# Performance work log

Hardware: AMD Instinct MI355X
Metric: run time of the kernel (lower is better)

The kernel has to match this reference:

```python
import jax, jax.numpy as jnp
import numpy as np

N_NODES, N_EDGES, D_FEAT, HIDDEN, N_CLASSES = 100000, 3200000, 128, 16, 40


def setup_inputs() -> dict:
    key = jax.random.key(0)
    ks = jax.random.split(key, 6)
    x = jax.random.normal(ks[0], (N_NODES, D_FEAT), dtype=jnp.float32)
    edge_index = jax.random.randint(ks[1], (2, N_EDGES), 0, N_NODES, dtype=jnp.int32)
    # SAGEConv params: lin_l (aggregated neighbors, with bias), lin_r (root, no bias)
    W_l = jax.random.normal(ks[2], (D_FEAT, HIDDEN), dtype=jnp.float32) / np.sqrt(D_FEAT)
    b_l = jnp.zeros((HIDDEN,), jnp.float32)
    W_r = jax.random.normal(ks[3], (D_FEAT, HIDDEN), dtype=jnp.float32) / np.sqrt(D_FEAT)
    # final Linear(hidden, num_classes)
    W3 = jax.random.normal(ks[4], (HIDDEN, N_CLASSES), dtype=jnp.float32) / np.sqrt(HIDDEN)
    b3 = jnp.zeros((N_CLASSES,), jnp.float32)
    return {"x": x, "edge_index": edge_index, "W_l": W_l, "b_l": b_l,
            "W_r": W_r, "W3": W3, "b3": b3}


def reference(x, edge_index, W_l, b_l, W_r, W3, b3):
    N = x.shape[0]
    src, dst = edge_index[0], edge_index[1]
    # mean aggregation of source features onto target nodes (PyG source_to_target)
    agg = jax.ops.segment_sum(x[src], dst, num_segments=N)            # [N, F]
    deg = jax.ops.segment_sum(jnp.ones_like(dst, dtype=x.dtype), dst, num_segments=N)
    mean = agg / jnp.maximum(deg, 1.0)[:, None]                        # zero-in-degree -> 0
    # SAGEConv: lin_l(mean) + lin_r(x)
    h = mean @ W_l + b_l + x @ W_r                                     # [N, 16]
    h = jax.nn.relu(h)
    logits = h @ W3 + b3                                               # [N, C]
    return jax.nn.log_softmax(logits, axis=1)
```

## Files before the change

### kernel.cpp

```cpp
#include <hip/hip_runtime.h>
#include <hip/hip_bf16.h>

#define D_FEAT 128
#define HIDDEN 16
#define NCLS 40
#define EPB 4096
#define QSCALE 32.0f
#define QBIAS  8.0f

typedef unsigned int uint;

__device__ __forceinline__ void fma4(float4& a, float s, const float4 w) {
  a.x += s * w.x; a.y += s * w.y; a.z += s * w.z; a.w += s * w.w;
}

__global__ __launch_bounds__(256) void pass1_kernel(
    const int* __restrict__ src, const int* __restrict__ dst,
    int* __restrict__ gcur1, int* __restrict__ buf1,
    int E, int C, int R1) {
  __shared__ int lh[32], loff[32], gbase[32];
  __shared__ int lbuf[EPB];
  __shared__ int ldst[EPB];
  int tid = threadIdx.x;
  if (tid < 32) lh[tid] = 0;
  __syncthreads();

  int base = blockIdx.x * EPB;
  int key[16], rnk[16], rec[16];
#pragma unroll
  for (int j = 0; j < 16; ++j) {
    int e = base + j * 256 + tid;
    bool ok = e < E;
    int d = ok ? dst[e] : 0;
    int s = ok ? src[e] : 0;
    key[j] = ok ? (d >> 12) : -1;
    rec[j] = s | ((d & 4095) << 17);
    if (ok) rnk[j] = atomicAdd(&lh[key[j]], 1);
  }
  __syncthreads();

  if (tid < 64) {
    int v = (tid < 32) ? lh[tid] : 0;
    int inc = v;
#pragma unroll
    for (int dd = 1; dd < 32; dd <<= 1) {
      int t = __shfl_up(inc, dd);
      if ((int)tid >= dd) inc += t;
    }
    if (tid < 32) {
      loff[tid] = inc - v;
      gbase[tid] = (v && tid < C) ? atomicAdd(&gcur1[tid], v) : 0;
    }
  }
  __syncthreads();

#pragma unroll
  for (int j = 0; j < 16; ++j) {
    if (key[j] >= 0) {
      int p = loff[key[j]] + rnk[j];
      lbuf[p] = rec[j];
      int gp = gbase[key[j]] + rnk[j];
      ldst[p] = (gp < R1) ? key[j] * R1 + gp : -1;
    }
  }
  __syncthreads();

  int tot = min(EPB, E - base);
  for (int i = tid; i < tot; i += 256) {
    int di = ldst[i];
    if (di >= 0) buf1[di] = lbuf[i];
  }
}

__global__ __launch_bounds__(256) void p2lin_kernel(
    const int* __restrict__ buf1, const int* __restrict__ gcur1,
    int* __restrict__ gcur, int* __restrict__ packed,
    int C, int R1, int RF, int chunks, int nb2,
    const float* __restrict__ x,
    const float* __restrict__ Wl, const float* __restrict__ Wr,
    uint* __restrict__ ylb, float* __restrict__ yr, int N) {
  __shared__ __align__(16) char smem[16896];
  int tid = threadIdx.x;

  if ((int)blockIdx.x < nb2) {
    int* lbuf  = (int*)smem;
    int* lh    = (int*)(smem + 16384);
    int* loff  = lh + 32;
    int* gbase = loff + 32;

    int c = blockIdx.x / chunks;
    int chunk = blockIdx.x - c * chunks;
    int cnt1 = min(gcur1[c], R1);
    int base = chunk * EPB;
    int tot = cnt1 - base;
    if (tot <= 0) return;
    tot = min(tot, EPB);

    if (tid < 32) lh[tid] = 0;
    __syncthreads();

    const int* in = buf1 + (size_t)c * R1 + base;
    int key[16], rnk[16], rec[16];
#pragma unroll
    for (int j = 0; j < 16; ++j) {
      int i = j * 256 + tid;
      bool ok = i < tot;
      int r = ok ? in[i] : 0;
      key[j] = ok ? ((r >> 24) & 31) : -1;
      rec[j] = r;
      if (ok) rnk[j] = atomicAdd(&lh[key[j]], 1);
    }
    __syncthreads();

    if (tid < 64) {
      int v = (tid < 32) ? lh[tid] : 0;
      int inc = v;
#pragma unroll
      for (int dd = 1; dd < 32; dd <<= 1) {
        int t = __shfl_up(inc, dd);
        if ((int)tid >= dd) inc += t;
      }
      if (tid < 32) {
        loff[tid] = inc - v;
        gbase[tid] = v ? atomicAdd(&gcur[c * 32 + tid], v) : 0;
      }
    }
    __syncthreads();

#pragma unroll
    for (int j = 0; j < 16; ++j)
      if (key[j] >= 0) lbuf[loff[key[j]] + rnk[j]] = rec[j];
    __syncthreads();

    for (int i = tid; i < tot; i += 256) {
      int r = lbuf[i];
      int k = (r >> 24) & 31;
      int gp = gbase[k] + (i - loff[k]);
      if (gp < RF) {
        int d12 = (r >> 17) & 4095;
        packed[(size_t)(c * 32 + k) * RF + gp] =
            (r & 0x1FFFF) | ((d12 & 127) << 20);
      }
    }
  } else {
    float* sW = (float*)smem;
    const float4* sWf4 = (const float4*)smem;

    for (int i = tid; i < 4096; i += 256) {
      int k = i >> 5, c = i & 31;
      sW[i] = (c < 16) ? Wl[k * 16 + c] : Wr[k * 16 + (c - 16)];
    }
    __syncthreads();

    int row0 = ((int)blockIdx.x - nb2) * 128;
    int quad = tid & 7, rg = tid >> 3;
    int r0 = row0 + rg * 4;
    int rr0 = min(r0 + 0, N - 1), rr1 = min(r0 + 1, N - 1);
    int rr2 = min(r0 + 2, N - 1), rr3 = min(r0 + 3, N - 1);
    const float* xp0 = x + (size_t)rr0 * D_FEAT;
    const float* xp1 = x + (size_t)rr1 * D_FEAT;
    const float* xp2 = x + (size_t)rr2 * D_FEAT;
    const float* xp3 = x + (size_t)rr3 * D_FEAT;

    float4 acc0 = {0,0,0,0}, acc1 = {0,0,0,0}, acc2 = {0,0,0,0}, acc3 = {0,0,0,0};
#pragma unroll 4
    for (int k4 = 0; k4 < 32; ++k4) {
      float4 x0 = *(const float4*)(xp0 + k4 * 4);
      float4 x1 = *(const float4*)(xp1 + k4 * 4);
      float4 x2 = *(const float4*)(xp2 + k4 * 4);
      float4 x3 = *(const float4*)(xp3 + k4 * 4);
      float4 w0 = sWf4[(k4 * 4 + 0) * 8 + quad];
      fma4(acc0, x0.x, w0); fma4(acc1, x1.x, w0);
      fma4(acc2, x2.x, w0); fma4(acc3, x3.x, w0);
      float4 w1 = sWf4[(k4 * 4 + 1) * 8 + quad];
      fma4(acc0, x0.y, w1); fma4(acc1, x1.y, w1);
      fma4(acc2, x2.y, w1); fma4(acc3, x3.y, w1);
      float4 w2 = sWf4[(k4 * 4 + 2) * 8 + quad];
      fma4(acc0, x0.z, w2); fma4(acc1, x1.z, w2);
      fma4(acc2, x2.z, w2); fma4(acc3, x3.z, w2);
      float4 w3 = sWf4[(k4 * 4 + 3) * 8 + quad];
      fma4(acc0, x0.w, w3); fma4(acc1, x1.w, w3);
      fma4(acc2, x2.w, w3); fma4(acc3, x3.w, w3);
    }

    float4 accs[4] = {acc0, acc1, acc2, acc3};
    if (quad < 4) {
#pragma unroll
      for (int r = 0; r < 4; ++r) {
        if (r0 + r < N) {
          float4 a = accs[r];
          int q0 = __float2int_rn((fminf(fmaxf(a.x, -7.9f), 7.9f) + QBIAS) * QSCALE);
          int q1 = __float2int_rn((fminf(fmaxf(a.y, -7.9f), 7.9f) + QBIAS) * QSCALE);
          int q2 = __float2int_rn((fminf(fmaxf(a.z, -7.9f), 7.9f) + QBIAS) * QSCALE);
          int q3 = __float2int_rn((fminf(fmaxf(a.w, -7.9f), 7.9f) + QBIAS) * QSCALE);
          uint2 pk;
          pk.x = (uint)q0 | ((uint)q1 << 16);
          pk.y = (uint)q2 | ((uint)q3 << 16);
          *(uint2*)(ylb + (size_t)(r0 + r) * 8 + quad * 2) = pk;
        }
      }
    } else {
#pragma unroll
      for (int r = 0; r < 4; ++r) {
        if (r0 + r < N)
          *(float4*)(yr + (size_t)(r0 + r) * 16 + (quad - 4) * 4) = accs[r];
      }
    }
  }
}

__global__ __launch_bounds__(1024) void baggrf_kernel(
    const uint* __restrict__ ylb, const int* __restrict__ packed,
    const int* __restrict__ gcur, const float* __restrict__ yr,
    const float* __restrict__ bl, const float* __restrict__ W3,
    const float* __restrict__ b3, float* __restrict__ out,
    int N, int RF) {
  __shared__ uint sagg[128 * 9];
  __shared__ int sdeg[128];
  __shared__ float syr[128 * 16];
  __shared__ float sW3[16 * NCLS];
  __shared__ float sb3[NCLS];
  __shared__ float sbl[16];
  int tid = threadIdx.x;
  int b = blockIdx.x;
  int node0 = b * 128;

  for (int i = tid; i < 128 * 9; i += 1024) sagg[i] = 0u;
  if (tid < 128) sdeg[tid] = 0;
  if (tid >= 384 && tid < 1024) sW3[tid - 384] = W3[tid - 384];
  if (tid < NCLS) sb3[tid] = b3[tid];
  if (tid >= 64 && tid < 80) sbl[tid - 64] = bl[tid - 64];
  __syncthreads();

  int cnt = min(gcur[b], RF);
  int lo = b * RF, hi = lo + cnt;
  for (int e = lo + tid; e < hi; e += 2048) {
    int eb = e + 1024;
    bool has2 = eb < hi;
    int p0 = packed[e];
    int p1 = packed[has2 ? eb : e];
    int s0 = p0 & 0xFFFFF, d0 = (p0 >> 20) & 127;
    int s1 = p1 & 0xFFFFF, d1 = (p1 >> 20) & 127;
    const uint4* q0 = (const uint4*)(ylb + (size_t)s0 * 8);
    const uint4* q1 = (const uint4*)(ylb + (size_t)s1 * 8);
    uint4 a0 = q0[0], a1 = q0[1];
    uint4 b0 = q1[0], b1 = q1[1];

    uint* ip0 = &sagg[d0 * 9];
    atomicAdd(ip0 + 0, a0.x); atomicAdd(ip0 + 1, a0.y);
    atomicAdd(ip0 + 2, a0.z); atomicAdd(ip0 + 3, a0.w);
    atomicAdd(ip0 + 4, a1.x); atomicAdd(ip0 + 5, a1.y);
    atomicAdd(ip0 + 6, a1.z); atomicAdd(ip0 + 7, a1.w);
    atomicAdd(&sdeg[d0], 1);
    if (has2) {
      uint* ip1 = &sagg[d1 * 9];
      atomicAdd(ip1 + 0, b0.x); atomicAdd(ip1 + 1, b0.y);
      atomicAdd(ip1 + 2, b0.z); atomicAdd(ip1 + 3, b0.w);
      atomicAdd(ip1 + 4, b1.x); atomicAdd(ip1 + 5, b1.y);
      atomicAdd(ip1 + 6, b1.z); atomicAdd(ip1 + 7, b1.w);
      atomicAdd(&sdeg[d1], 1);
    }
  }

  int nvalid = min(128, N - node0);
  if (nvalid > 0) {
    int tot16 = nvalid * 16;
    for (int i = tid; i < tot16; i += 1024)
      syr[i] = yr[(size_t)node0 * 16 + i];
  }
  __syncthreads();

  int node = tid >> 3, q = tid & 7;
  int n = node0 + node;
  if (n < N) {
    int dg = sdeg[node];
    float bsub = (QBIAS * QSCALE) * (float)dg;
    float inv = 1.0f / (QSCALE * fmaxf((float)dg, 1.0f));
    float h[16];
#pragma unroll
    for (int j = 0; j < 8; ++j) {
      uint s = sagg[node * 9 + j];
      float v0 = ((float)(s & 0xFFFFu) - bsub) * inv;
      float v1 = ((float)(s >> 16) - bsub) * inv;
      h[2 * j]     = fmaxf(v0 + sbl[2 * j]     + syr[node * 16 + 2 * j], 0.f);
      h[2 * j + 1] = fmaxf(v1 + sbl[2 * j + 1] + syr[node * 16 + 2 * j + 1], 0.f);
    }
    float lg[5];
#pragma unroll
    for (int j = 0; j < 5; ++j) lg[j] = sb3[q * 5 + j];
#pragma unroll
    for (int k = 0; k < 16; ++k) {
      float hv = h[k];
#pragma unroll
      for (int j = 0; j < 5; ++j) lg[j] += hv * sW3[k * NCLS + q * 5 + j];
    }
    float m = lg[0];
#pragma unroll
    for (int j = 1; j < 5; ++j) m = fmaxf(m, lg[j]);
#pragma unroll
    for (int dd = 1; dd < 8; dd <<= 1) m = fmaxf(m, __shfl_xor(m, dd));
    float s = 0.f;
#pragma unroll
    for (int j = 0; j < 5; ++j) s += __expf(lg[j] - m);
#pragma unroll
    for (int dd = 1; dd < 8; dd <<= 1) s += __shfl_xor(s, dd);
    float lse = m + __logf(s);
    float* op = out + (size_t)n * NCLS + q * 5;
#pragma unroll
    for (int j = 0; j < 5; ++j) op[j] = lg[j] - lse;
  }
}

extern "C" void kernel_launch(void* const* d_in, const int* in_sizes, int n_in,
                              void* d_out, int out_size, void* d_ws, size_t ws_size,
                              hipStream_t stream) {
  const float* x   = (const float*)d_in[0];
  const int* eidx  = (const int*)d_in[1];
  const float* Wl  = (const float*)d_in[2];
  const float* bl  = (const float*)d_in[3];
  const float* Wr  = (const float*)d_in[4];
  const float* W3  = (const float*)d_in[5];
  const float* b3  = (const float*)d_in[6];
  float* out = (float*)d_out;

  int N = in_sizes[0] / D_FEAT;
  int E = in_sizes[1] / 2;
  const int* src = eidx;
  const int* dst = eidx + E;

  int C = (N + 4095) >> 12;
  int chunks = (E / C) / EPB + 2;
  int R1 = chunks * EPB;
  int Bf = C * 32;
  int B = (N + 127) >> 7;
  long long m = (long long)E * 128 / N;
  int RF = (int)((m + m / 8 + 511) / 512 * 512);

  size_t n16 = (size_t)N * 16;
  uint* ylb   = (uint*)d_ws;
  float* yr   = (float*)(ylb + (size_t)N * 8);
  int* gcur   = (int*)(yr + n16);
  int* gcur1  = gcur + Bf;
  int* buf1   = gcur1 + C;
  int* packed = buf1 + (size_t)C * R1;

  hipMemsetAsync(gcur, 0, (size_t)(Bf + C) * sizeof(int), stream);

  int nb1 = (E + EPB - 1) / EPB;
  pass1_kernel<<<nb1, 256, 0, stream>>>(src, dst, gcur1, buf1, E, C, R1);

  int nb2 = C * chunks;
  int nblin = (N + 127) / 128;
  p2lin_kernel<<<nb2 + nblin, 256, 0, stream>>>(buf1, gcur1, gcur, packed,
                                                C, R1, RF, chunks, nb2,
                                                x, Wl, Wr, ylb, yr, N);

  baggrf_kernel<<<B, 1024, 0, stream>>>(ylb, packed, gcur, yr, bl, W3, b3,
                                        out, N, RF);
}
```

Before: 97.83 us.

## Co-schedule linear projection with pass1 sort and unroll aggregation loop to four edges

Moves the dense x@W projection blocks out of the pass-2 launch and into the pass-1 bucketing launch, so the projection runs alongside the first radix partition rather than the second. Pass 1 now keeps each record's bucket key in a byte array in shared memory, which cuts its shared-memory footprint from two EPB int arrays. The final aggregation loop now handles four edges per thread per iteration instead of two, giving more outstanding gathers. The costs are higher register pressure in the aggregation kernel and a different per-kernel balance across the three launches.

```diff
diff --git a/kernel.cpp b/kernel.cpp
--- a/kernel.cpp
+++ b/kernel.cpp
@@ -14,100 +14,35 @@
   a.x += s * w.x; a.y += s * w.y; a.z += s * w.z; a.w += s * w.w;
 }
 
-__global__ __launch_bounds__(256) void pass1_kernel(
+__global__ __launch_bounds__(256) void p1lin_kernel(
     const int* __restrict__ src, const int* __restrict__ dst,
     int* __restrict__ gcur1, int* __restrict__ buf1,
-    int E, int C, int R1) {
-  __shared__ int lh[32], loff[32], gbase[32];
-  __shared__ int lbuf[EPB];
-  __shared__ int ldst[EPB];
-  int tid = threadIdx.x;
-  if (tid < 32) lh[tid] = 0;
-  __syncthreads();
-
-  int base = blockIdx.x * EPB;
-  int key[16], rnk[16], rec[16];
-#pragma unroll
-  for (int j = 0; j < 16; ++j) {
-    int e = base + j * 256 + tid;
-    bool ok = e < E;
-    int d = ok ? dst[e] : 0;
-    int s = ok ? src[e] : 0;
-    key[j] = ok ? (d >> 12) : -1;
-    rec[j] = s | ((d & 4095) << 17);
-    if (ok) rnk[j] = atomicAdd(&lh[key[j]], 1);
-  }
-  __syncthreads();
-
-  if (tid < 64) {
-    int v = (tid < 32) ? lh[tid] : 0;
-    int inc = v;
-#pragma unroll
-    for (int dd = 1; dd < 32; dd <<= 1) {
-      int t = __shfl_up(inc, dd);
-      if ((int)tid >= dd) inc += t;
-    }
-    if (tid < 32) {
-      loff[tid] = inc - v;
-      gbase[tid] = (v && tid < C) ? atomicAdd(&gcur1[tid], v) : 0;
-    }
-  }
-  __syncthreads();
-
-#pragma unroll
-  for (int j = 0; j < 16; ++j) {
-    if (key[j] >= 0) {
-      int p = loff[key[j]] + rnk[j];
-      lbuf[p] = rec[j];
-      int gp = gbase[key[j]] + rnk[j];
-      ldst[p] = (gp < R1) ? key[j] * R1 + gp : -1;
-    }
-  }
-  __syncthreads();
-
-  int tot = min(EPB, E - base);
-  for (int i = tid; i < tot; i += 256) {
-    int di = ldst[i];
-    if (di >= 0) buf1[di] = lbuf[i];
-  }
-}
-
-__global__ __launch_bounds__(256) void p2lin_kernel(
-    const int* __restrict__ buf1, const int* __restrict__ gcur1,
-    int* __restrict__ gcur, int* __restrict__ packed,
-    int C, int R1, int RF, int chunks, int nb2,
+    int E, int C, int R1, int nb1,
     const float* __restrict__ x,
     const float* __restrict__ Wl, const float* __restrict__ Wr,
     uint* __restrict__ ylb, float* __restrict__ yr, int N) {
-  __shared__ __align__(16) char smem[16896];
+  __shared__ __align__(16) char smem[20880];
   int tid = threadIdx.x;
 
-  if ((int)blockIdx.x < nb2) {
+  if ((int)blockIdx.x < nb1) {
     int* lbuf  = (int*)smem;
-    int* lh    = (int*)(smem + 16384);
+    unsigned char* skey = (unsigned char*)(smem + 16384);
+    int* lh    = (int*)(smem + 20480);
     int* loff  = lh + 32;
-    int* gbase = loff + 32;
-
-    int c = blockIdx.x / chunks;
-    int chunk = blockIdx.x - c * chunks;
-    int cnt1 = min(gcur1[c], R1);
-    int base = chunk * EPB;
-    int tot = cnt1 - base;
-    if (tot <= 0) return;
-    tot = min(tot, EPB);
-
+    int* gbase = loff + 33;
     if (tid < 32) lh[tid] = 0;
     __syncthreads();
 
-    const int* in = buf1 + (size_t)c * R1 + base;
+    int base = blockIdx.x * EPB;
     int key[16], rnk[16], rec[16];
 #pragma unroll
     for (int j = 0; j < 16; ++j) {
-      int i = j * 256 + tid;
-      bool ok = i < tot;
-      int r = ok ? in[i] : 0;
-      key[j] = ok ? ((r >> 24) & 31) : -1;
-      rec[j] = r;
+      int e = base + j * 256 + tid;
+      bool ok = e < E;
+      int d = ok ? dst[e] : 0;
+      int s = ok ? src[e] : 0;
+      key[j] = ok ? (d >> 12) : -1;
+      rec[j] = s | ((d & 4095) << 17);
       if (ok) rnk[j] = atomicAdd(&lh[key[j]], 1);
     }
     __syncthreads();
@@ -122,25 +57,27 @@
       }
       if (tid < 32) {
         loff[tid] = inc - v;
-        gbase[tid] = v ? atomicAdd(&gcur[c * 32 + tid], v) : 0;
-      }
-    }
-    __syncthreads();
-
-#pragma unroll
-    for (int j = 0; j < 16; ++j)
-      if (key[j] >= 0) lbuf[loff[key[j]] + rnk[j]] = rec[j];
-    __syncthreads();
-
+        gbase[tid] = (v && tid < C) ? atomicAdd(&gcur1[tid], v) : 0;
+      }
+    }
+    __syncthreads();
+
+#pragma unroll
+    for (int j = 0; j < 16; ++j) {
+      if (key[j] >= 0) {
+        int p = loff[key[j]] + rnk[j];
+        lbuf[p] = rec[j];
+        skey[p] = (unsigned char)key[j];
+      }
+    }
+    __syncthreads();
+
+    int tot = min(EPB, E - base);
     for (int i = tid; i < tot; i += 256) {
       int r = lbuf[i];
-      int k = (r >> 24) & 31;
+      int k = skey[i];
       int gp = gbase[k] + (i - loff[k]);
-      if (gp < RF) {
-        int d12 = (r >> 17) & 4095;
-        packed[(size_t)(c * 32 + k) * RF + gp] =
-            (r & 0x1FFFF) | ((d12 & 127) << 20);
-      }
+      if (gp < R1) buf1[(size_t)k * R1 + gp] = r;
     }
   } else {
     float* sW = (float*)smem;
@@ -152,7 +89,7 @@
     }
     __syncthreads();
 
-    int row0 = ((int)blockIdx.x - nb2) * 128;
+    int row0 = ((int)blockIdx.x - nb1) * 128;
     int quad = tid & 7, rg = tid >> 3;
     int r0 = row0 + rg * 4;
     int rr0 = min(r0 + 0, N - 1), rr1 = min(r0 + 1, N - 1);
@@ -209,6 +146,70 @@
   }
 }
 
+__global__ __launch_bounds__(256) void pass2_kernel(
+    const int* __restrict__ buf1, const int* __restrict__ gcur1,
+    int* __restrict__ gcur, int* __restrict__ packed,
+    int C, int R1, int RF, int chunks) {
+  __shared__ int lbuf[EPB];
+  __shared__ int lh[32], loff[32], gbase[32];
+
+  int c = blockIdx.x / chunks;
+  int chunk = blockIdx.x - c * chunks;
+  int cnt1 = min(gcur1[c], R1);
+  int base = chunk * EPB;
+  int tot = cnt1 - base;
+  if (tot <= 0) return;
+  tot = min(tot, EPB);
+
+  int tid = threadIdx.x;
+  if (tid < 32) lh[tid] = 0;
+  __syncthreads();
+
+  const int* in = buf1 + (size_t)c * R1 + base;
+  int key[16], rnk[16], rec[16];
+#pragma unroll
+  for (int j = 0; j < 16; ++j) {
+    int i = j * 256 + tid;
+    bool ok = i < tot;
+    int r = ok ? in[i] : 0;
+    key[j] = ok ? ((r >> 24) & 31) : -1;
+    rec[j] = r;
+    if (ok) rnk[j] = atomicAdd(&lh[key[j]], 1);
+  }
+  __syncthreads();
+
+  if (tid < 64) {
+    int v = (tid < 32) ? lh[tid] : 0;
+    int inc = v;
+#pragma unroll
+    for (int dd = 1; dd < 32; dd <<= 1) {
+      int t = __shfl_up(inc, dd);
+      if ((int)tid >= dd) inc += t;
+    }
+    if (tid < 32) {
+      loff[tid] = inc - v;
+      gbase[tid] = v ? atomicAdd(&gcur[c * 32 + tid], v) : 0;
+    }
+  }
+  __syncthreads();
+
+#pragma unroll
+  for (int j = 0; j < 16; ++j)
+    if (key[j] >= 0) lbuf[loff[key[j]] + rnk[j]] = rec[j];
+  __syncthreads();
+
+  for (int i = tid; i < tot; i += 256) {
+    int r = lbuf[i];
+    int k = (r >> 24) & 31;
+    int gp = gbase[k] + (i - loff[k]);
+    if (gp < RF) {
+      int d12 = (r >> 17) & 4095;
+      packed[(size_t)(c * 32 + k) * RF + gp] =
+          (r & 0x1FFFF) | ((d12 & 127) << 20);
+    }
+  }
+}
+
 __global__ __launch_bounds__(1024) void baggrf_kernel(
     const uint* __restrict__ ylb, const int* __restrict__ packed,
     const int* __restrict__ gcur, const float* __restrict__ yr,
@@ -234,17 +235,25 @@
 
   int cnt = min(gcur[b], RF);
   int lo = b * RF, hi = lo + cnt;
-  for (int e = lo + tid; e < hi; e += 2048) {
-    int eb = e + 1024;
-    bool has2 = eb < hi;
-    int p0 = packed[e];
-    int p1 = packed[has2 ? eb : e];
+  for (int e0 = lo + tid; e0 < hi; e0 += 4096) {
+    int e1 = e0 + 1024, e2 = e0 + 2048, e3 = e0 + 3072;
+    bool h1 = e1 < hi, h2 = e2 < hi, h3 = e3 < hi;
+    int p0 = packed[e0];
+    int p1 = packed[h1 ? e1 : e0];
+    int p2 = packed[h2 ? e2 : e0];
+    int p3 = packed[h3 ? e3 : e0];
     int s0 = p0 & 0xFFFFF, d0 = (p0 >> 20) & 127;
     int s1 = p1 & 0xFFFFF, d1 = (p1 >> 20) & 127;
+    int s2 = p2 & 0xFFFFF, d2 = (p2 >> 20) & 127;
+    int s3 = p3 & 0xFFFFF, d3 = (p3 >> 20) & 127;
     const uint4* q0 = (const uint4*)(ylb + (size_t)s0 * 8);
     const uint4* q1 = (const uint4*)(ylb + (size_t)s1 * 8);
+    const uint4* q2 = (const uint4*)(ylb + (size_t)s2 * 8);
+    const uint4* q3 = (const uint4*)(ylb + (size_t)s3 * 8);
     uint4 a0 = q0[0], a1 = q0[1];
     uint4 b0 = q1[0], b1 = q1[1];
+    uint4 c0 = q2[0], c1 = q2[1];
+    uint4 e4 = q3[0], e5 = q3[1];
 
     uint* ip0 = &sagg[d0 * 9];
     atomicAdd(ip0 + 0, a0.x); atomicAdd(ip0 + 1, a0.y);
@@ -252,13 +261,29 @@
     atomicAdd(ip0 + 4, a1.x); atomicAdd(ip0 + 5, a1.y);
     atomicAdd(ip0 + 6, a1.z); atomicAdd(ip0 + 7, a1.w);
     atomicAdd(&sdeg[d0], 1);
-    if (has2) {
-      uint* ip1 = &sagg[d1 * 9];
-      atomicAdd(ip1 + 0, b0.x); atomicAdd(ip1 + 1, b0.y);
-      atomicAdd(ip1 + 2, b0.z); atomicAdd(ip1 + 3, b0.w);
-      atomicAdd(ip1 + 4, b1.x); atomicAdd(ip1 + 5, b1.y);
-      atomicAdd(ip1 + 6, b1.z); atomicAdd(ip1 + 7, b1.w);
+    if (h1) {
+      uint* ip = &sagg[d1 * 9];
+      atomicAdd(ip + 0, b0.x); atomicAdd(ip + 1, b0.y);
+      atomicAdd(ip + 2, b0.z); atomicAdd(ip + 3, b0.w);
+      atomicAdd(ip + 4, b1.x); atomicAdd(ip + 5, b1.y);
+      atomicAdd(ip + 6, b1.z); atomicAdd(ip + 7, b1.w);
       atomicAdd(&sdeg[d1], 1);
+    }
+    if (h2) {
+      uint* ip = &sagg[d2 * 9];
+      atomicAdd(ip + 0, c0.x); atomicAdd(ip + 1, c0.y);
+      atomicAdd(ip + 2, c0.z); atomicAdd(ip + 3, c0.w);
+      atomicAdd(ip + 4, c1.x); atomicAdd(ip + 5, c1.y);
+      atomicAdd(ip + 6, c1.z); atomicAdd(ip + 7, c1.w);
+      atomicAdd(&sdeg[d2], 1);
+    }
+    if (h3) {
+      uint* ip = &sagg[d3 * 9];
+      atomicAdd(ip + 0, e4.x); atomicAdd(ip + 1, e4.y);
+      atomicAdd(ip + 2, e4.z); atomicAdd(ip + 3, e4.w);
+      atomicAdd(ip + 4, e5.x); atomicAdd(ip + 5, e5.y);
+      atomicAdd(ip + 6, e5.z); atomicAdd(ip + 7, e5.w);
+      atomicAdd(&sdeg[d3], 1);
     }
   }
 
@@ -347,13 +372,13 @@
   hipMemsetAsync(gcur, 0, (size_t)(Bf + C) * sizeof(int), stream);
 
   int nb1 = (E + EPB - 1) / EPB;
-  pass1_kernel<<<nb1, 256, 0, stream>>>(src, dst, gcur1, buf1, E, C, R1);
-
-  int nb2 = C * chunks;
   int nblin = (N + 127) / 128;
-  p2lin_kernel<<<nb2 + nblin, 256, 0, stream>>>(buf1, gcur1, gcur, packed,
-                                                C, R1, RF, chunks, nb2,
+  p1lin_kernel<<<nb1 + nblin, 256, 0, stream>>>(src, dst, gcur1, buf1,
+                                                E, C, R1, nb1,
                                                 x, Wl, Wr, ylb, yr, N);
+
+  pass2_kernel<<<C * chunks, 256, 0, stream>>>(buf1, gcur1, gcur, packed,
+                                               C, R1, RF, chunks);
 
   baggrf_kernel<<<B, 1024, 0, stream>>>(ylb, packed, gcur, yr, bl, W3, b3,
                                         out, N, RF);
```

After: 98.86 us. No clear change (+1.0%).
